# Kernel tuning notes

Hardware: AMD Instinct MI355X
Metric: run time of the kernel (lower is better)

## Reference

```python
import jax, jax.numpy as jnp
import numpy as np
import math

N = 50000      # nodes
E = 800000     # edges
IN = 64        # in_channels
HID = 128      # hidden_channels
OUT = 64       # out_channels
RATIO = 0.8
K = int(math.ceil(RATIO * N))  # 40000 nodes kept after TopKPooling


def setup_inputs() -> dict:
    key = jax.random.key(0)
    ks = jax.random.split(key, 12)
    x = jax.random.normal(ks[0], (N, IN), jnp.float32)
    edge_index = jax.random.randint(ks[1], (2, E), 0, N, dtype=jnp.int32)
    batch = jnp.zeros((N,), jnp.int32)  # single graph

    def glorot(k, fi, fo):
        return jax.random.normal(k, (fi, fo), jnp.float32) * (1.0 / np.sqrt(fi))

    W1 = glorot(ks[2], IN, HID);  b1 = jnp.zeros((HID,), jnp.float32)
    pool_w = jax.random.normal(ks[3], (HID,), jnp.float32) * (1.0 / np.sqrt(HID))
    W2 = glorot(ks[4], HID, OUT); b2 = jnp.zeros((OUT,), jnp.float32)
    W3 = glorot(ks[5], OUT, HID); b3 = jnp.zeros((HID,), jnp.float32)
    W4 = glorot(ks[6], HID, IN);  b4 = jnp.zeros((IN,), jnp.float32)
    return dict(x=x, edge_index=edge_index, batch=batch,
                W1=W1, b1=b1, pool_w=pool_w, W2=W2, b2=b2,
                W3=W3, b3=b3, W4=W4, b4=b4)


def gcn_conv(x, src, dst, ew, W, b, n):
    """PyG GCNConv: D^{-1/2}(A+I)D^{-1/2} X W + b; ew is a 0/1 edge mask."""
    h = x @ W                                             # [n, d_out]
    deg = 1.0 + jax.ops.segment_sum(ew, dst, num_segments=n)  # self-loop adds 1
    dis = jax.lax.rsqrt(deg)
    norm = dis[src] * dis[dst] * ew                       # [E]
    agg = jax.ops.segment_sum(norm[:, None] * h[src], dst, num_segments=n)
    agg = agg + h * (dis * dis)[:, None]                  # self-loop: norm = 1/deg
    return agg + b


def reference(x, edge_index, batch, W1, b1, pool_w, W2, b2, W3, b3, W4, b4):
    src, dst = edge_index[0], edge_index[1]
    ew = jnp.ones((E,), x.dtype)

    # conv1 + relu
    h = jax.nn.relu(gcn_conv(x, src, dst, ew, W1, b1, N))

    # TopKPooling(ratio=0.8): score = tanh(x.w/||w||), keep top-K, scale x by score
    score = jnp.tanh(h @ pool_w / jnp.linalg.norm(pool_w))  # [N]
    vals, perm = jax.lax.top_k(score, K)
    hp = h[perm] * vals[:, None]                            # [K, HID]
    # remap edges to pooled node ids; drop edges touching removed nodes via mask
    new_idx = jnp.full((N,), -1, jnp.int32).at[perm].set(jnp.arange(K, dtype=jnp.int32))
    ns, nd = new_idx[src], new_idx[dst]
    valid = ((ns >= 0) & (nd >= 0)).astype(x.dtype)
    ns = jnp.maximum(ns, 0)
    nd = jnp.maximum(nd, 0)

    h2 = jax.nn.relu(gcn_conv(hp, ns, nd, valid, W2, b2, K))
    h3 = jax.nn.relu(gcn_conv(h2, ns, nd, valid, W3, b3, K))
    h4 = gcn_conv(h3, ns, nd, valid, W4, b4, K)             # [K, IN]

    # global_mean_pool over the (single) graph -> [1, IN]
    return jnp.mean(h4, axis=0, keepdims=True)
```

## Files before the change

### kernel.cpp

```cpp
#include <hip/hip_runtime.h>
#include <hip/hip_bf16.h>
#include <stdint.h>

#define N_NODES 50000
#define N_EDGES 800000
#define K_KEEP  40000
#define BKT     196
#define BCAP    6144

typedef unsigned long long u64;
typedef unsigned int u32;
typedef unsigned short u16;
typedef __hip_bfloat16 bf16;
typedef __hip_bfloat162 bf16x2;
typedef __attribute__((ext_vector_type(8))) short short8;
typedef __attribute__((ext_vector_type(8))) unsigned short ushort8;
typedef __attribute__((ext_vector_type(4))) float f32x4;

struct Ctl {
  u64 prefix;
  u32 kremain;
  u32 cnt;
  float inv_norm;
  u32 isfp32;
  u32 done;
  u32 pad;
  u32 gen;
  u32 done2;
  u32 hist[256];
};

__device__ __forceinline__ float bf2f(bf16 v) { return __bfloat162float(v); }
__device__ __forceinline__ float bfbits2f(unsigned short u) {
  return __uint_as_float(((u32)u) << 16);
}
__device__ __forceinline__ float loadF(const void* p, size_t i, bool f32) {
  return f32 ? ((const float*)p)[i] : bf2f(((const bf16*)p)[i]);
}
__device__ __forceinline__ short f2bf_bits(float f) {
  bf16 t = __float2bfloat16(f);
  return *(const short*)&t;
}

__device__ __forceinline__ void gather_row8_pre(const ushort8* __restrict__ H, int d, int lane,
                                                const int* __restrict__ rowstart,
                                                const int* __restrict__ len,
                                                const int* __restrict__ csr,
                                                float* acc)
{
  ushort8 v = H[(size_t)d * 8 + lane];
  #pragma unroll
  for (int c = 0; c < 8; ++c) acc[c] = bfbits2f(v[c]);
  int i = rowstart[d];
  int i1 = len ? (i + len[d]) : rowstart[d + 1];
  for (; i + 8 <= i1; i += 8) {
    int s0 = csr[i],     s1 = csr[i + 1], s2 = csr[i + 2], s3 = csr[i + 3];
    int s4 = csr[i + 4], s5 = csr[i + 5], s6 = csr[i + 6], s7 = csr[i + 7];
    ushort8 v0 = H[(size_t)s0 * 8 + lane];
    ushort8 v1 = H[(size_t)s1 * 8 + lane];
    ushort8 v2 = H[(size_t)s2 * 8 + lane];
    ushort8 v3 = H[(size_t)s3 * 8 + lane];
    ushort8 v4 = H[(size_t)s4 * 8 + lane];
    ushort8 v5 = H[(size_t)s5 * 8 + lane];
    ushort8 v6 = H[(size_t)s6 * 8 + lane];
    ushort8 v7 = H[(size_t)s7 * 8 + lane];
    #pragma unroll
    for (int c = 0; c < 8; ++c) {
      acc[c] += (bfbits2f(v0[c]) + bfbits2f(v1[c]))
              + (bfbits2f(v2[c]) + bfbits2f(v3[c]));
      acc[c] += (bfbits2f(v4[c]) + bfbits2f(v5[c]))
              + (bfbits2f(v6[c]) + bfbits2f(v7[c]));
    }
  }
  for (; i + 4 <= i1; i += 4) {
    int s0 = csr[i], s1 = csr[i + 1], s2 = csr[i + 2], s3 = csr[i + 3];
    ushort8 v0 = H[(size_t)s0 * 8 + lane];
    ushort8 v1 = H[(size_t)s1 * 8 + lane];
    ushort8 v2 = H[(size_t)s2 * 8 + lane];
    ushort8 v3 = H[(size_t)s3 * 8 + lane];
    #pragma unroll
    for (int c = 0; c < 8; ++c) {
      acc[c] += (bfbits2f(v0[c]) + bfbits2f(v1[c]))
              + (bfbits2f(v2[c]) + bfbits2f(v3[c]));
    }
  }
  for (; i < i1; ++i) {
    int s = csr[i];
    ushort8 vv = H[(size_t)s * 8 + lane];
    #pragma unroll
    for (int c = 0; c < 8; ++c) acc[c] += bfbits2f(vv[c]);
  }
}

__device__ __forceinline__ void gather_wave_partial(const ushort8* __restrict__ H, int d,
                                                    int slot, int unit,
                                                    const int* __restrict__ rowstart,
                                                    const int* __restrict__ len,
                                                    const int* __restrict__ csr,
                                                    float* acc)
{
  #pragma unroll
  for (int c = 0; c < 8; ++c) acc[c] = 0.f;
  if (slot == 0) {
    ushort8 v = H[(size_t)d * 8 + unit];
    #pragma unroll
    for (int c = 0; c < 8; ++c) acc[c] = bfbits2f(v[c]);
  }
  int i0 = rowstart[d];
  int i1 = i0 + len[d];
  int i = i0 + slot;
  for (; i + 8 < i1; i += 16) {
    int sa = csr[i], sb = csr[i + 8];
    ushort8 va = H[(size_t)sa * 8 + unit];
    ushort8 vb = H[(size_t)sb * 8 + unit];
    #pragma unroll
    for (int c = 0; c < 8; ++c) acc[c] += bfbits2f(va[c]) + bfbits2f(vb[c]);
  }
  if (i < i1) {
    int s = csr[i];
    ushort8 vv = H[(size_t)s * 8 + unit];
    #pragma unroll
    for (int c = 0; c < 8; ++c) acc[c] += bfbits2f(vv[c]);
  }
}


__global__ void init_kernel(const unsigned short* __restrict__ x16,
                            int* __restrict__ bucket_cur, int* __restrict__ detcnt, Ctl* ctl) {
  __shared__ u32 dsh[256];
  int i = blockIdx.x * 256 + threadIdx.x;
  if (i < BKT) bucket_cur[i] = i * BCAP;
  if (blockIdx.x == 0) {
    ctl->hist[threadIdx.x] = 0u;
    if (threadIdx.x == 0) {
      ctl->prefix = 0ull; ctl->kremain = K_KEEP; ctl->cnt = 0u;
      ctl->done = 0u; ctl->pad = 0u; ctl->gen = 0u; ctl->done2 = 0u;
    }
  }
  if (blockIdx.x < 64) {
    int base = blockIdx.x * 2048;
    u32 c = 0;
    for (int j = threadIdx.x; j < 2048; j += 256) {
      u32 h = x16[base + j];
      if ((h & 0x7F80u) == 0x7F80u) c++;
    }
    dsh[threadIdx.x] = c;
    __syncthreads();
    for (int s = 128; s > 0; s >>= 1) {
      if (threadIdx.x < s) dsh[threadIdx.x] += dsh[threadIdx.x + s];
      __syncthreads();
    }
    if (threadIdx.x == 0) detcnt[blockIdx.x] = (int)dsh[0];
  }
}


__global__ void bucket_scatter_kernel(const int* __restrict__ src, const int* __restrict__ dst,
                                      int* __restrict__ bucket_cur, u32* __restrict__ bucketbuf,
                                      const int* __restrict__ detcnt, const void* __restrict__ pw,
                                      Ctl* ctl)
{
  __shared__ u32 hist[BKT];
  __shared__ u32 base[BKT];
  __shared__ int f32sh;
  __shared__ float ns[128];
  const int tid = threadIdx.x;
  const int e0 = blockIdx.x * 2048;

  if (tid < 64) {
    int dc = detcnt[tid];
    for (int off = 32; off; off >>= 1) dc += __shfl_down(dc, off);
    if (tid == 0) f32sh = (dc >= 16) ? 1 : 0;
  }
  for (int t = tid; t < BKT; t += 256) hist[t] = 0;
  __syncthreads();
  const bool f32in = f32sh != 0;

  int dreg[8], sreg[8];
  #pragma unroll
  for (int j = 0; j < 8; ++j) {
    int e = e0 + j * 256 + tid;
    if (e < N_EDGES) { dreg[j] = dst[e]; sreg[j] = src[e]; }
    else             { dreg[j] = -1;     sreg[j] = 0;      }
  }
  #pragma unroll
  for (int j = 0; j < 8; ++j)
    if (dreg[j] >= 0) atomicAdd(&hist[dreg[j] >> 8], 1u);
  __syncthreads();
  for (int t = tid; t < BKT; t += 256) {
    u32 c = hist[t];
    base[t] = c ? (u32)atomicAdd(&bucket_cur[t], (int)c) : 0u;
    hist[t] = 0;
  }
  __syncthreads();
  #pragma unroll
  for (int j = 0; j < 8; ++j) {
    if (dreg[j] >= 0) {
      int d = dreg[j];
      int b = d >> 8;
      u32 pos = base[b] + atomicAdd(&hist[b], 1u);
      bucketbuf[pos] = ((u32)sreg[j] << 8) | (u32)(d & 255);
    }
  }
  if (blockIdx.x == 0) {
    if (tid < 128) { float v = loadF(pw, tid, f32in); ns[tid] = v * v; }
    __syncthreads();
    for (int s = 64; s > 0; s >>= 1) {
      if (tid < s) ns[tid] += ns[tid + s];
      __syncthreads();
    }
    if (tid == 0) {
      ctl->inv_norm = 1.0f / sqrtf(ns[0]);
      ctl->isfp32 = f32in ? 1u : 0u;
    }
  }
}


__global__ void csr_from_buckets_kernel(const u32* __restrict__ bucketbuf, const int* __restrict__ bucket_cur,
                                        int* __restrict__ rowstart, float* __restrict__ dis,
                                        int* __restrict__ csr,
                                        const void* __restrict__ x, ushort8* __restrict__ xbf,
                                        const Ctl* __restrict__ ctl)
{
  __shared__ u32 cnt[256];
  __shared__ u32 loc[256];
  __shared__ u32 cur[256];
  __shared__ float disS[256];
  const int b = blockIdx.x;
  const int tid = threadIdx.x;

  int v = (tid < BKT) ? (bucket_cur[tid] - tid * BCAP) : 0;
  loc[tid] = (u32)v;
  __syncthreads();
  for (int off = 1; off < 256; off <<= 1) {
    u32 t = (tid >= off) ? loc[tid - off] : 0;
    __syncthreads();
    loc[tid] += t;
    __syncthreads();
  }
  const int bc = bucket_cur[b] - b * BCAP;
  const int off0 = (int)loc[b] - bc;
  if (b == BKT - 1 && tid == 0) rowstart[N_NODES] = (int)loc[BKT - 1];
  __syncthreads();

  const u32* buf = bucketbuf + (size_t)b * BCAP;
  cnt[tid] = 0;
  __syncthreads();
  for (int i = tid; i < bc; i += 256) atomicAdd(&cnt[buf[i] & 255u], 1u);
  __syncthreads();
  u32 c = cnt[tid];
  loc[tid] = c;
  __syncthreads();
  for (int off = 1; off < 256; off <<= 1) {
    u32 t = (tid >= off) ? loc[tid - off] : 0;
    __syncthreads();
    loc[tid] += t;
    __syncthreads();
  }
  int node = b * 256 + tid;
  u32 excl = loc[tid] - c;
  float ddv = rsqrtf(1.0f + (float)c);
  disS[tid] = ddv;
  if (node < N_NODES) {
    rowstart[node] = off0 + (int)excl;
    dis[node] = ddv;
  }
  cur[tid] = off0 + excl;
  __syncthreads();
  for (int i = tid; i < bc; i += 256) {
    u32 p = buf[i];
    u32 pos = atomicAdd(&cur[p & 255u], 1u);
    csr[pos] = (int)(p >> 8);
  }
  {
    const bool f32in = ctl->isfp32 != 0;
    if (f32in) {
      const float* xf = (const float*)x;
      for (int u = tid; u < 2048; u += 256) {
        int r = u >> 3, lane = u & 7;
        int d = b * 256 + r;
        if (d < N_NODES) {
          float sc = disS[r];
          ushort8 o;
          #pragma unroll
          for (int c2 = 0; c2 < 8; ++c2)
            o[c2] = (u16)f2bf_bits(xf[(size_t)d * 64 + lane * 8 + c2] * sc);
          xbf[(size_t)d * 8 + lane] = o;
        }
      }
    } else {
      const ushort8* xi = (const ushort8*)x;
      for (int u = tid; u < 2048; u += 256) {
        int r = u >> 3, lane = u & 7;
        int d = b * 256 + r;
        if (d < N_NODES) {
          float sc = disS[r];
          ushort8 vv = xi[(size_t)d * 8 + lane];
          ushort8 o;
          #pragma unroll
          for (int c2 = 0; c2 < 8; ++c2)
            o[c2] = (u16)f2bf_bits(bfbits2f(vv[c2]) * sc);
          xbf[(size_t)d * 8 + lane] = o;
        }
      }
    }
  }
}


__global__ void gather_h2_kernel(const bf16* __restrict__ P, const int* __restrict__ rowstart,
                                 const int* __restrict__ len, const int* __restrict__ csr,
                                 const float* __restrict__ dis,
                                 const void* __restrict__ b, const Ctl* __restrict__ ctl,
                                 bf16* __restrict__ P2, int M)
{
  const bool f32 = ctl->isfp32 != 0;
  const int tid = threadIdx.x;
  const int d = blockIdx.x * 4 + (tid >> 6);
  const int lane = tid & 63;
  const int slot = lane >> 3, unit = lane & 7;
  const ushort8* H = (const ushort8*)P;
  float acc[8];
  gather_wave_partial(H, d, slot, unit, rowstart, len, csr, acc);
  #pragma unroll
  for (int m = 8; m < 64; m <<= 1)
    #pragma unroll
    for (int c = 0; c < 8; ++c) acc[c] += __shfl_xor(acc[c], m);
  if (slot == 0) {
    float dd = dis[d];
    ushort8 outv;
    #pragma unroll
    for (int c = 0; c < 8; ++c) {
      float h = acc[c] * dd + loadF(b, 8 * unit + c, f32);
      outv[c] = (u16)f2bf_bits(fmaxf(h, 0.f) * dd);
    }
    ((ushort8*)P2)[(size_t)d * 8 + unit] = outv;
  }
}


__global__ void gemm_in_kernel(const ushort8* __restrict__ xbf,
                               const int* __restrict__ rowstart, const int* __restrict__ csr,
                               const float* __restrict__ dis,
                               const void* __restrict__ W, const void* __restrict__ b,
                               const void* __restrict__ pw,
                               bf16* __restrict__ Y, const Ctl* __restrict__ ctl,
                               float* __restrict__ score, u64* __restrict__ keys)
{
  __shared__ short Xs[64 * 72];
  __shared__ short Wt[128 * 72];
  __shared__ float bs[128];
  __shared__ float ps[128];
  const bool f32 = ctl->isfp32 != 0;
  const int tid = threadIdx.x;
  const int row0 = blockIdx.x * 64;

  if (!f32) {
    const short8* W8 = (const short8*)W;
    for (int i = tid; i < 1024; i += 256) {
      int k = i >> 4, nb = i & 15;
      short8 v = W8[i];
      #pragma unroll
      for (int j = 0; j < 8; ++j) Wt[(nb * 8 + j) * 72 + k] = v[j];
    }
  } else {
    for (int i = tid; i < 64 * 128; i += 256) {
      int k = i >> 7, n = i & 127;
      Wt[n * 72 + k] = f2bf_bits(((const float*)W)[i]);
    }
  }
  for (int u = tid; u < 512; u += 256) {
    int r = u >> 3, lane = u & 7;
    int d = row0 + r;
    float acc[8];
    short8 outv;
    if (d < N_NODES) {
      gather_row8_pre(xbf, d, lane, rowstart, nullptr, csr, acc);
      float dd = dis[d];
      #pragma unroll
      for (int c = 0; c < 8; ++c) outv[c] = f2bf_bits(acc[c] * dd);
    } else {
      #pragma unroll
      for (int c = 0; c < 8; ++c) outv[c] = 0;
    }
    *(short8*)&Xs[r * 72 + lane * 8] = outv;
  }
  for (int i = tid; i < 128; i += 256) { bs[i] = loadF(b, i, f32); ps[i] = loadF(pw, i, f32); }
  __syncthreads();

  const int lane = tid & 63;
  const int w = tid >> 6;
  const int l16 = lane & 15;
  const int quad = lane >> 4;
  f32x4 acc[8];
  #pragma unroll
  for (int ct = 0; ct < 8; ++ct) acc[ct] = (f32x4){0.f, 0.f, 0.f, 0.f};
  const int arow = w * 16 + l16;
  #pragma unroll
  for (int kc = 0; kc < 2; ++kc) {
    short8 a = *(short8*)&Xs[arow * 72 + kc * 32 + quad * 8];
    #pragma unroll
    for (int ct = 0; ct < 8; ++ct) {
      short8 bb = *(short8*)&Wt[(ct * 16 + l16) * 72 + kc * 32 + quad * 8];
      acc[ct] = __builtin_amdgcn_mfma_f32_16x16x32_bf16(a, bb, acc[ct], 0, 0, 0);
    }
  }
  float inv_norm = ctl->inv_norm;
  #pragma unroll
  for (int r = 0; r < 4; ++r) {
    int gr = row0 + w * 16 + quad * 4 + r;
    float p = 0.f;
    #pragma unroll
    for (int ct = 0; ct < 8; ++ct) {
      int col = ct * 16 + l16;
      float h = acc[ct][r] + bs[col];
      if (gr < N_NODES) Y[(size_t)gr * 128 + col] = __float2bfloat16(h);
      p += fmaxf(h, 0.f) * ps[col];
    }
    p += __shfl_down(p, 8, 16);
    p += __shfl_down(p, 4, 16);
    p += __shfl_down(p, 2, 16);
    p += __shfl_down(p, 1, 16);
    if (l16 == 0 && gr < N_NODES) {
      float sc = tanhf(p * inv_norm);
      score[gr] = sc;
      u32 u = __float_as_uint(sc);
      u = (u & 0x80000000u) ? ~u : (u | 0x80000000u);
      keys[gr] = (((u64)u) << 16) | (u64)(0xFFFFu - (u32)gr);
    }
  }
}

__global__ void gemm_128_64_kernel(const bf16* __restrict__ X, const void* __restrict__ W,
                                   bf16* __restrict__ Y, const Ctl* __restrict__ ctl,
                                   int M, int relu_x,
                                   const int* __restrict__ kept, const float* __restrict__ score,
                                   const float* __restrict__ prescale)
{
  __shared__ short Xs[64 * 136];
  __shared__ short Wt[64 * 136];
  __shared__ int keptS[64];
  __shared__ float scS[64];
  const bool f32 = ctl->isfp32 != 0;
  const int tid = threadIdx.x;
  const int row0 = blockIdx.x * 64;

  if (kept) {
    for (int i = tid; i < 64; i += 256) {
      int o = kept[row0 + i];
      keptS[i] = o;
      scS[i] = score[o];
    }
  }
  __syncthreads();

  if (!f32) {
    const short8* W8 = (const short8*)W;
    for (int i = tid; i < 1024; i += 256) {
      int k = i >> 3, nb = i & 7;
      short8 v = W8[i];
      #pragma unroll
      for (int j = 0; j < 8; ++j) Wt[(nb * 8 + j) * 136 + k] = v[j];
    }
  } else {
    for (int i = tid; i < 128 * 64; i += 256) {
      int k = i >> 6, n = i & 63;
      Wt[n * 136 + k] = f2bf_bits(((const float*)W)[i]);
    }
  }
  const u32* X2 = (const u32*)X;
  for (int p = tid; p < 64 * 64; p += 256) {
    int r = p >> 6, kp = p & 63;
    int srow = kept ? keptS[r] : (row0 + r);
    u32 v = X2[(size_t)srow * 64 + kp];
    if (relu_x) {
      if (v & 0x8000u) v &= 0xFFFF0000u;
      if (v & 0x80000000u) v &= 0x0000FFFFu;
    }
    if (kept) {
      bf16x2 h = *(bf16x2*)&v;
      float s = scS[r];
      bf16x2 o;
      o.x = __float2bfloat16(fmaxf(bf2f(h.x), 0.f) * s);
      o.y = __float2bfloat16(fmaxf(bf2f(h.y), 0.f) * s);
      v = *(u32*)&o;
    }
    *(u32*)&Xs[r * 136 + 2 * kp] = v;
  }
  __syncthreads();

  const int lane = tid & 63;
  const int w = tid >> 6;
  const int l16 = lane & 15;
  const int quad = lane >> 4;
  f32x4 acc[4];
  #pragma unroll
  for (int ct = 0; ct < 4; ++ct) acc[ct] = (f32x4){0.f, 0.f, 0.f, 0.f};
  const int arow = w * 16 + l16;
  #pragma unroll
  for (int kc = 0; kc < 4; ++kc) {
    short8 a = *(short8*)&Xs[arow * 136 + kc * 32 + quad * 8];
    #pragma unroll
    for (int ct = 0; ct < 4; ++ct) {
      short8 bb = *(short8*)&Wt[(ct * 16 + l16) * 136 + kc * 32 + quad * 8];
      acc[ct] = __builtin_amdgcn_mfma_f32_16x16x32_bf16(a, bb, acc[ct], 0, 0, 0);
    }
  }
  #pragma unroll
  for (int ct = 0; ct < 4; ++ct)
    #pragma unroll
    for (int r = 0; r < 4; ++r) {
      int gr = row0 + w * 16 + quad * 4 + r;
      float val = acc[ct][r];
      if (prescale) val *= prescale[gr];
      Y[(size_t)gr * 64 + ct * 16 + l16] = __float2bfloat16(val);
    }
}

__global__ void gemm_64_128_kernel(const bf16* __restrict__ P2,
                                   const int* __restrict__ rowstart, const int* __restrict__ len,
                                   const int* __restrict__ csr, const float* __restrict__ dis,
                                   const void* __restrict__ W, const void* __restrict__ b,
                                   bf16* __restrict__ Y, const Ctl* __restrict__ ctl, int M)
{
  __shared__ short Xs[64 * 72];
  __shared__ short Wt[128 * 72];
  __shared__ float bs[128];
  const bool f32 = ctl->isfp32 != 0;
  const int tid = threadIdx.x;
  const int row0 = blockIdx.x * 64;

  if (!f32) {
    const short8* W8 = (const short8*)W;
    for (int i = tid; i < 1024; i += 256) {
      int k = i >> 4, nb = i & 15;
      short8 v = W8[i];
      #pragma unroll
      for (int j = 0; j < 8; ++j) Wt[(nb * 8 + j) * 72 + k] = v[j];
    }
  } else {
    for (int i = tid; i < 64 * 128; i += 256) {
      int k = i >> 7, n = i & 127;
      Wt[n * 72 + k] = f2bf_bits(((const float*)W)[i]);
    }
  }
  {
    const ushort8* H = (const ushort8*)P2;
    for (int u = tid; u < 512; u += 256) {
      int r = u >> 3, lane = u & 7;
      int d = row0 + r;
      float acc[8];
      gather_row8_pre(H, d, lane, rowstart, len, csr, acc);
      float dd = dis[d];
      short8 outv;
      #pragma unroll
      for (int c = 0; c < 8; ++c) outv[c] = f2bf_bits(acc[c] * dd);
      *(short8*)&Xs[r * 72 + lane * 8] = outv;
    }
  }
  for (int i = tid; i < 128; i += 256) bs[i] = loadF(b, i, f32);
  __syncthreads();

  const int lane = tid & 63;
  const int w = tid >> 6;
  const int l16 = lane & 15;
  const int quad = lane >> 4;
  f32x4 acc[8];
  #pragma unroll
  for (int ct = 0; ct < 8; ++ct) acc[ct] = (f32x4){0.f, 0.f, 0.f, 0.f};
  const int arow = w * 16 + l16;
  #pragma unroll
  for (int kc = 0; kc < 2; ++kc) {
    short8 a = *(short8*)&Xs[arow * 72 + kc * 32 + quad * 8];
    #pragma unroll
    for (int ct = 0; ct < 8; ++ct) {
      short8 bb = *(short8*)&Wt[(ct * 16 + l16) * 72 + kc * 32 + quad * 8];
      acc[ct] = __builtin_amdgcn_mfma_f32_16x16x32_bf16(a, bb, acc[ct], 0, 0, 0);
    }
  }
  #pragma unroll
  for (int ct = 0; ct < 8; ++ct)
    #pragma unroll
    for (int r = 0; r < 4; ++r) {
      int gr = row0 + w * 16 + quad * 4 + r;
      int col = ct * 16 + l16;
      Y[(size_t)gr * 128 + col] = __float2bfloat16(acc[ct][r] + bs[col]);
    }
}

__global__ void agg_gather64_final_kernel(const bf16* __restrict__ P, const int* __restrict__ rowstart,
                                          const int* __restrict__ len, const int* __restrict__ csr,
                                          const float* __restrict__ dis,
                                          float* __restrict__ partial, int M, int nblk)
{
  __shared__ float cs[64];
  const int tid = threadIdx.x;
  if (tid < 64) cs[tid] = 0.f;
  __syncthreads();
  const int lane = tid & 63;
  const int slot = lane >> 3, unit = lane & 7;
  const int wave = tid >> 6;
  const ushort8* H = (const ushort8*)P;
  float acc[8];
  #pragma unroll
  for (int c = 0; c < 8; ++c) acc[c] = 0.f;
  for (int d = blockIdx.x * 4 + wave; d < M; d += nblk * 4) {
    float part[8];
    gather_wave_partial(H, d, slot, unit, rowstart, len, csr, part);
    float dd = dis[d];
    #pragma unroll
    for (int c = 0; c < 8; ++c) acc[c] += part[c] * dd;
  }
  #pragma unroll
  for (int c = 0; c < 8; ++c) atomicAdd(&cs[8 * unit + c], acc[c]);
  __syncthreads();
  if (tid < 64) partial[(size_t)tid * nblk + blockIdx.x] = cs[tid];
}

__global__ void reduce_out_kernel(const float* __restrict__ partial, const void* __restrict__ b,
                                  const Ctl* __restrict__ ctl, void* __restrict__ out, int nblk)
{
  __shared__ float sh[256];
  int c = blockIdx.x;
  float s = 0.f;
  for (int j = threadIdx.x; j < nblk; j += 256) s += partial[(size_t)c * nblk + j];
  sh[threadIdx.x] = s;
  __syncthreads();
  for (int st = 128; st > 0; st >>= 1) {
    if (threadIdx.x < st) sh[threadIdx.x] += sh[threadIdx.x + st];
    __syncthreads();
  }
  if (threadIdx.x == 0) {
    const bool f32 = ctl->isfp32 != 0;
    float val = sh[0] / (float)K_KEEP + loadF(b, c, f32);
    if (f32) ((float*)out)[c] = val;
    else     ((bf16*)out)[c] = __float2bfloat16(val);
  }
}


__device__ __forceinline__ void mark_slice(const u64* __restrict__ keys, Ctl* ctl,
                                           int* __restrict__ new_idx, int* __restrict__ kept,
                                           int i)
{
  if (i >= N_NODES) return;
  if (keys[i] >= ctl->prefix) {
    int pos = (int)atomicAdd(&ctl->cnt, 1u);
    new_idx[i] = pos;
    kept[pos] = i;
  } else {
    new_idx[i] = -1;
  }
}

__global__ void histpick_kernel(const u64* __restrict__ keys, Ctl* ctl, int shift, int pass,
                                int nblocks, int* __restrict__ new_idx, int* __restrict__ kept) {
  __shared__ u32 lh[256];
  __shared__ u32 sfx[256];
  __shared__ int lastflag;
  __shared__ int selsh;
  const int tid = threadIdx.x;
  const u32 g = ctl->gen;
  if (g != 0u) {
    if ((u32)pass == g)
      mark_slice(keys, ctl, new_idx, kept, blockIdx.x * 256 + tid);
    return;
  }
  lh[tid] = 0;
  __syncthreads();
  u64 prefix = ctl->prefix;
  int i = blockIdx.x * 256 + tid;
  if (i < N_NODES) {
    u64 key = keys[i];
    if ((key >> (shift + 8)) == (prefix >> (shift + 8)))
      atomicAdd(&lh[(u32)((key >> shift) & 0xFF)], 1u);
  }
  __syncthreads();
  u32 c = lh[tid];
  if (c) atomicAdd(&ctl->hist[tid], c);
  __syncthreads();
  if (tid == 0) {
    __threadfence();
    u32 old = atomicAdd(&ctl->done, 1u);
    lastflag = (old == (u32)(nblocks - 1));
  }
  __syncthreads();
  if (!lastflag) return;
  u32 cc = atomicExch(&ctl->hist[tid], 0u);
  sfx[tid] = cc;
  __syncthreads();
  for (int off = 1; off < 256; off <<= 1) {
    u32 t = (tid + off < 256) ? sfx[tid + off] : 0u;
    __syncthreads();
    sfx[tid] += t;
    __syncthreads();
  }
  u32 kr = ctl->kremain;
  u32 above = (tid < 255) ? sfx[tid + 1] : 0u;
  if (sfx[tid] >= kr && above < kr) selsh = tid;
  __syncthreads();
  if (tid == 0) {
    int sel = selsh;
    u32 ab = (sel < 255) ? sfx[sel + 1] : 0u;
    u32 newkr = kr - ab;
    u32 bucketcnt = sfx[sel] - ab;
    ctl->kremain = newkr;
    ctl->prefix = prefix | (((u64)(u32)sel) << shift);
    if (newkr == bucketcnt) ctl->gen = (u32)(pass + 1);
    ctl->done = 0u;
  }
}

__global__ void mark_kernel(const u64* __restrict__ keys, Ctl* ctl,
                            int* __restrict__ new_idx, int* __restrict__ kept)
{
  u32 g = ctl->gen;
  if (g >= 1u && g <= 5u) return;
  mark_slice(keys, ctl, new_idx, kept, blockIdx.x * 256 + (int)threadIdx.x);
}


__global__ void csr2_build_kernel(const int* __restrict__ kept, const int* __restrict__ rowstart1,
                                  const int* __restrict__ csr1, const int* __restrict__ new_idx,
                                  Ctl* ctl, int* __restrict__ rowstart2, int* __restrict__ len2,
                                  float* __restrict__ dis2, int* __restrict__ csr2)
{
  int kp = blockIdx.x * 256 + threadIdx.x;
  int lane = threadIdx.x & 63;
  int c = 0;
  int i0 = 0, i1 = 0;
  if (kp < K_KEEP) {
    int o = kept[kp];
    i0 = rowstart1[o]; i1 = rowstart1[o + 1];
    int i = i0;
    for (; i + 4 <= i1; i += 4) {
      int s0 = csr1[i], s1 = csr1[i + 1], s2 = csr1[i + 2], s3 = csr1[i + 3];
      c += (new_idx[s0] >= 0) + (new_idx[s1] >= 0) + (new_idx[s2] >= 0) + (new_idx[s3] >= 0);
    }
    for (; i < i1; ++i) c += (new_idx[csr1[i]] >= 0);
  }
  int pre = c;
  #pragma unroll
  for (int off = 1; off < 64; off <<= 1) {
    int t = __shfl_up(pre, off);
    if (lane >= off) pre += t;
  }
  int wtot = __shfl(pre, 63);
  int wbase = 0;
  if (lane == 0) wbase = (int)atomicAdd(&ctl->pad, (u32)wtot);
  wbase = __shfl(wbase, 0);
  int base = wbase + pre - c;
  if (kp < K_KEEP) {
    rowstart2[kp] = base;
    len2[kp] = c;
    dis2[kp] = rsqrtf(1.0f + (float)c);
    int w = base;
    for (int i = i0; i < i1; ++i) {
      int ns = new_idx[csr1[i]];
      if (ns >= 0) csr2[w++] = ns;
    }
  }
}


extern "C" void kernel_launch(void* const* d_in, const int* in_sizes, int n_in,
                              void* d_out, int out_size, void* d_ws, size_t ws_size,
                              hipStream_t stream)
{
  const void* x  = d_in[0];
  const int*  ei = (const int*)d_in[1];
  const void* W1 = d_in[3];
  const void* b1 = d_in[4];
  const void* pw = d_in[5];
  const void* W2 = d_in[6];
  const void* b2 = d_in[7];
  const void* W3 = d_in[8];
  const void* b3 = d_in[9];
  const void* W4 = d_in[10];
  const void* b4 = d_in[11];

  const int* src = ei;
  const int* dst = ei + N_EDGES;

  float* F = (float*)d_ws;
  bf16*  A16       = (bf16*)F;
  bf16*  B16       = (bf16*)(F + 3200000);
  bf16*  C16       = (bf16*)(F + 6400000);
  u32*   xbf       = (u32*)(F + 9000000);
  float* dis1      = F + 10600000;
  float* dis2      = F + 10650000;
  float* score     = F + 10690000;
  u64*   keys      = (u64*)(F + 10740000);
  int*   new_idx   = (int*)(F + 10840000);
  int*   kept      = (int*)(F + 10890000);
  int*   len2      = (int*)(F + 10930000);
  int*   rowstart1 = (int*)(F + 10970000);
  int*   rowstart2 = (int*)(F + 11020004);
  int*   csr1      = (int*)(F + 11060008);
  int*   csr2      = (int*)(F + 11860008);
  Ctl*   ctl       = (Ctl*)(F + 12660008);
  int*   detcnt    = (int*)(F + 12660856);
  int*   bucket_cur= (int*)(F + 12660920);
  u32*   bucketbuf = (u32*)(F + 12726908);
  float* partial   = F + 13931132;

  const int NB1 = (N_NODES + 255) / 256;
  const int EB2 = (N_EDGES + 2047) / 2048;
  const int GB1 = (N_NODES + 63) / 64;
  const int WBK = K_KEEP / 4;
  const int CB2 = (K_KEEP + 255) / 256;
  const int NBF = 1024;

  init_kernel<<<NB1, 256, 0, stream>>>((const unsigned short*)x, bucket_cur, detcnt, ctl);

  bucket_scatter_kernel<<<EB2, 256, 0, stream>>>(src, dst, bucket_cur, bucketbuf,
                                                 detcnt, pw, ctl);
  csr_from_buckets_kernel<<<BKT, 256, 0, stream>>>(bucketbuf, bucket_cur, rowstart1, dis1, csr1,
                                                   x, (ushort8*)xbf, ctl);

  gemm_in_kernel<<<GB1, 256, 0, stream>>>((const ushort8*)xbf, rowstart1, csr1, dis1,
                                          W1, b1, pw, B16, ctl, score, keys);

  for (int p = 0; p < 6; ++p)
    histpick_kernel<<<NB1, 256, 0, stream>>>(keys, ctl, 40 - 8 * p, p, NB1, new_idx, kept);
  mark_kernel<<<NB1, 256, 0, stream>>>(keys, ctl, new_idx, kept);

  csr2_build_kernel<<<CB2, 256, 0, stream>>>(kept, rowstart1, csr1, new_idx, ctl,
                                             rowstart2, len2, dis2, csr2);

  gemm_128_64_kernel<<<K_KEEP / 64, 256, 0, stream>>>(B16, W2, A16, ctl, K_KEEP, 0, kept, score, dis2);
  gather_h2_kernel<<<WBK, 256, 0, stream>>>(A16, rowstart2, len2, csr2, dis2, b2, ctl, C16, K_KEEP);

  gemm_64_128_kernel<<<K_KEEP / 64, 256, 0, stream>>>(C16, rowstart2, len2, csr2, dis2,
                                                      W3, b3, B16, ctl, K_KEEP);

  gemm_128_64_kernel<<<K_KEEP / 64, 256, 0, stream>>>(B16, W4, A16, ctl, K_KEEP, 1, nullptr, nullptr, dis2);
  agg_gather64_final_kernel<<<NBF, 256, 0, stream>>>(A16, rowstart2, len2, csr2, dis2,
                                                     partial, K_KEEP, NBF);
  reduce_out_kernel<<<64, 256, 0, stream>>>(partial, b4, ctl, d_out, NBF);
}
```

Measured before the change: 305.2 us.

## Use 12-bit radix passes for top-k selection and vectorize edge loads

```diff
diff --git a/kernel.cpp b/kernel.cpp
--- a/kernel.cpp
+++ b/kernel.cpp
@@ -7,6 +7,8 @@
 #define K_KEEP  40000
 #define BKT     196
 #define BCAP    6144
+#define RBITS   12
+#define RBINS   4096
 
 typedef unsigned long long u64;
 typedef unsigned int u32;
@@ -126,16 +128,15 @@
 
 
 __global__ void init_kernel(const unsigned short* __restrict__ x16,
-                            int* __restrict__ bucket_cur, int* __restrict__ detcnt, Ctl* ctl) {
+                            int* __restrict__ bucket_cur, int* __restrict__ detcnt,
+                            Ctl* ctl, u32* __restrict__ hist4k) {
   __shared__ u32 dsh[256];
   int i = blockIdx.x * 256 + threadIdx.x;
   if (i < BKT) bucket_cur[i] = i * BCAP;
-  if (blockIdx.x == 0) {
-    ctl->hist[threadIdx.x] = 0u;
-    if (threadIdx.x == 0) {
-      ctl->prefix = 0ull; ctl->kremain = K_KEEP; ctl->cnt = 0u;
-      ctl->done = 0u; ctl->pad = 0u; ctl->gen = 0u; ctl->done2 = 0u;
-    }
+  if (i < RBINS) hist4k[i] = 0u;
+  if (blockIdx.x == 0 && threadIdx.x == 0) {
+    ctl->prefix = 0ull; ctl->kremain = K_KEEP; ctl->cnt = 0u;
+    ctl->done = 0u; ctl->pad = 0u; ctl->gen = 0u; ctl->done2 = 0u;
   }
   if (blockIdx.x < 64) {
     int base = blockIdx.x * 2048;
@@ -177,11 +178,23 @@
   const bool f32in = f32sh != 0;
 
   int dreg[8], sreg[8];
-  #pragma unroll
-  for (int j = 0; j < 8; ++j) {
-    int e = e0 + j * 256 + tid;
-    if (e < N_EDGES) { dreg[j] = dst[e]; sreg[j] = src[e]; }
-    else             { dreg[j] = -1;     sreg[j] = 0;      }
+  const int eb = e0 + tid * 8;
+  if (e0 + 2048 <= N_EDGES) {
+    const int4* d4 = (const int4*)(dst + eb);
+    const int4* s4 = (const int4*)(src + eb);
+    int4 da = d4[0], db = d4[1];
+    int4 sa = s4[0], sb = s4[1];
+    dreg[0] = da.x; dreg[1] = da.y; dreg[2] = da.z; dreg[3] = da.w;
+    dreg[4] = db.x; dreg[5] = db.y; dreg[6] = db.z; dreg[7] = db.w;
+    sreg[0] = sa.x; sreg[1] = sa.y; sreg[2] = sa.z; sreg[3] = sa.w;
+    sreg[4] = sb.x; sreg[5] = sb.y; sreg[6] = sb.z; sreg[7] = sb.w;
+  } else {
+    #pragma unroll
+    for (int j = 0; j < 8; ++j) {
+      int e = eb + j;
+      if (e < N_EDGES) { dreg[j] = dst[e]; sreg[j] = src[e]; }
+      else             { dreg[j] = -1;     sreg[j] = 0;      }
+    }
   }
   #pragma unroll
   for (int j = 0; j < 8; ++j)
@@ -654,12 +667,12 @@
   }
 }
 
-__global__ void histpick_kernel(const u64* __restrict__ keys, Ctl* ctl, int shift, int pass,
-                                int nblocks, int* __restrict__ new_idx, int* __restrict__ kept) {
-  __shared__ u32 lh[256];
+__global__ void histpick_kernel(const u64* __restrict__ keys, Ctl* ctl, u32* __restrict__ hist4k,
+                                int shift, int pass, int nblocks,
+                                int* __restrict__ new_idx, int* __restrict__ kept) {
+  __shared__ u32 lh[RBINS];
   __shared__ u32 sfx[256];
   __shared__ int lastflag;
-  __shared__ int selsh;
   const int tid = threadIdx.x;
   const u32 g = ctl->gen;
   if (g != 0u) {
@@ -667,18 +680,21 @@
       mark_slice(keys, ctl, new_idx, kept, blockIdx.x * 256 + tid);
     return;
   }
-  lh[tid] = 0;
+  #pragma unroll
+  for (int j = 0; j < RBINS / 256; ++j) lh[tid + j * 256] = 0;
   __syncthreads();
   u64 prefix = ctl->prefix;
   int i = blockIdx.x * 256 + tid;
   if (i < N_NODES) {
     u64 key = keys[i];
-    if ((key >> (shift + 8)) == (prefix >> (shift + 8)))
-      atomicAdd(&lh[(u32)((key >> shift) & 0xFF)], 1u);
-  }
-  __syncthreads();
-  u32 c = lh[tid];
-  if (c) atomicAdd(&ctl->hist[tid], c);
+    if ((key >> (shift + RBITS)) == (prefix >> (shift + RBITS)))
+      atomicAdd(&lh[(u32)((key >> shift) & (RBINS - 1))], 1u);
+  }
+  __syncthreads();
+  for (int bb = tid; bb < RBINS; bb += 256) {
+    u32 c = lh[bb];
+    if (c) atomicAdd(&hist4k[bb], c);
+  }
   __syncthreads();
   if (tid == 0) {
     __threadfence();
@@ -687,8 +703,18 @@
   }
   __syncthreads();
   if (!lastflag) return;
-  u32 cc = atomicExch(&ctl->hist[tid], 0u);
-  sfx[tid] = cc;
+  u32 cnt[16];
+  u32 loc[16];
+  {
+    u32 tot = 0;
+    #pragma unroll
+    for (int j = 15; j >= 0; --j) {
+      cnt[j] = atomicExch(&hist4k[tid * 16 + j], 0u);
+      tot += cnt[j];
+      loc[j] = tot;
+    }
+    sfx[tid] = tot;
+  }
   __syncthreads();
   for (int off = 1; off < 256; off <<= 1) {
     u32 t = (tid + off < 256) ? sfx[tid + off] : 0u;
@@ -697,18 +723,19 @@
     __syncthreads();
   }
   u32 kr = ctl->kremain;
-  u32 above = (tid < 255) ? sfx[tid + 1] : 0u;
-  if (sfx[tid] >= kr && above < kr) selsh = tid;
-  __syncthreads();
-  if (tid == 0) {
-    int sel = selsh;
-    u32 ab = (sel < 255) ? sfx[sel + 1] : 0u;
-    u32 newkr = kr - ab;
-    u32 bucketcnt = sfx[sel] - ab;
-    ctl->kremain = newkr;
-    ctl->prefix = prefix | (((u64)(u32)sel) << shift);
-    if (newkr == bucketcnt) ctl->gen = (u32)(pass + 1);
-    ctl->done = 0u;
+  u32 above_chunks = (tid < 255) ? sfx[tid + 1] : 0u;
+  #pragma unroll
+  for (int j = 0; j < 16; ++j) {
+    u32 gs  = loc[j] + above_chunks;
+    u32 gs1 = ((j < 15) ? loc[j + 1] : 0u) + above_chunks;
+    if (gs >= kr && gs1 < kr) {
+      int sel = tid * 16 + j;
+      u32 newkr = kr - gs1;
+      ctl->kremain = newkr;
+      ctl->prefix = prefix | (((u64)(u32)sel) << shift);
+      if (newkr == cnt[j]) ctl->gen = (u32)(pass + 1);
+      ctl->done = 0u;
+    }
   }
 }
 
@@ -716,7 +743,7 @@
                             int* __restrict__ new_idx, int* __restrict__ kept)
 {
   u32 g = ctl->gen;
-  if (g >= 1u && g <= 5u) return;
+  if (g >= 1u && g <= 3u) return;
   mark_slice(keys, ctl, new_idx, kept, blockIdx.x * 256 + (int)threadIdx.x);
 }
 
@@ -802,6 +829,7 @@
   Ctl*   ctl       = (Ctl*)(F + 12660008);
   int*   detcnt    = (int*)(F + 12660856);
   int*   bucket_cur= (int*)(F + 12660920);
+  u32*   hist4k    = (u32*)(F + 12661120);
   u32*   bucketbuf = (u32*)(F + 12726908);
   float* partial   = F + 13931132;
 
@@ -812,7 +840,7 @@
   const int CB2 = (K_KEEP + 255) / 256;
   const int NBF = 1024;
 
-  init_kernel<<<NB1, 256, 0, stream>>>((const unsigned short*)x, bucket_cur, detcnt, ctl);
+  init_kernel<<<NB1, 256, 0, stream>>>((const unsigned short*)x, bucket_cur, detcnt, ctl, hist4k);
 
   bucket_scatter_kernel<<<EB2, 256, 0, stream>>>(src, dst, bucket_cur, bucketbuf,
                                                  detcnt, pw, ctl);
@@ -822,8 +850,9 @@
   gemm_in_kernel<<<GB1, 256, 0, stream>>>((const ushort8*)xbf, rowstart1, csr1, dis1,
                                           W1, b1, pw, B16, ctl, score, keys);
 
-  for (int p = 0; p < 6; ++p)
-    histpick_kernel<<<NB1, 256, 0, stream>>>(keys, ctl, 40 - 8 * p, p, NB1, new_idx, kept);
+  for (int p = 0; p < 4; ++p)
+    histpick_kernel<<<NB1, 256, 0, stream>>>(keys, ctl, hist4k, 36 - RBITS * p, p, NB1,
+                                             new_idx, kept);
   mark_kernel<<<NB1, 256, 0, stream>>>(keys, ctl, new_idx, kept);
 
   csr2_build_kernel<<<CB2, 256, 0, stream>>>(kept, rowstart1, csr1, new_idx, ctl,
```

Measured after the change: 307.2 us. No clear change (+0.6%).

## Collapse final GCN layer and mean pool into weighted column sum

Applied to the files above, without the earlier changes.

```diff
diff --git a/kernel.cpp b/kernel.cpp
--- a/kernel.cpp
+++ b/kernel.cpp
@@ -126,10 +126,12 @@
 
 
 __global__ void init_kernel(const unsigned short* __restrict__ x16,
-                            int* __restrict__ bucket_cur, int* __restrict__ detcnt, Ctl* ctl) {
+                            int* __restrict__ bucket_cur, int* __restrict__ detcnt,
+                            Ctl* ctl, float* __restrict__ cvec) {
   __shared__ u32 dsh[256];
   int i = blockIdx.x * 256 + threadIdx.x;
   if (i < BKT) bucket_cur[i] = i * BCAP;
+  if (i < K_KEEP) cvec[i] = 0.f;
   if (blockIdx.x == 0) {
     ctl->hist[threadIdx.x] = 0u;
     if (threadIdx.x == 0) {
@@ -177,11 +179,23 @@
   const bool f32in = f32sh != 0;
 
   int dreg[8], sreg[8];
-  #pragma unroll
-  for (int j = 0; j < 8; ++j) {
-    int e = e0 + j * 256 + tid;
-    if (e < N_EDGES) { dreg[j] = dst[e]; sreg[j] = src[e]; }
-    else             { dreg[j] = -1;     sreg[j] = 0;      }
+  const int eb = e0 + tid * 8;
+  if (e0 + 2048 <= N_EDGES) {
+    const int4* d4 = (const int4*)(dst + eb);
+    const int4* s4 = (const int4*)(src + eb);
+    int4 da = d4[0], db = d4[1];
+    int4 sa = s4[0], sb = s4[1];
+    dreg[0] = da.x; dreg[1] = da.y; dreg[2] = da.z; dreg[3] = da.w;
+    dreg[4] = db.x; dreg[5] = db.y; dreg[6] = db.z; dreg[7] = db.w;
+    sreg[0] = sa.x; sreg[1] = sa.y; sreg[2] = sa.z; sreg[3] = sa.w;
+    sreg[4] = sb.x; sreg[5] = sb.y; sreg[6] = sb.z; sreg[7] = sb.w;
+  } else {
+    #pragma unroll
+    for (int j = 0; j < 8; ++j) {
+      int e = eb + j;
+      if (e < N_EDGES) { dreg[j] = dst[e]; sreg[j] = src[e]; }
+      else             { dreg[j] = -1;     sreg[j] = 0;      }
+    }
   }
   #pragma unroll
   for (int j = 0; j < 8; ++j)
@@ -589,53 +603,51 @@
     }
 }
 
-__global__ void agg_gather64_final_kernel(const bf16* __restrict__ P, const int* __restrict__ rowstart,
-                                          const int* __restrict__ len, const int* __restrict__ csr,
-                                          const float* __restrict__ dis,
-                                          float* __restrict__ partial, int M, int nblk)
-{
-  __shared__ float cs[64];
+
+__global__ void weighted_sum_kernel(const bf16* __restrict__ H3, const float* __restrict__ cvec,
+                                    const float* __restrict__ dis,
+                                    float* __restrict__ partial, int M, int nblk)
+{
+  __shared__ float cs[128];
   const int tid = threadIdx.x;
-  if (tid < 64) cs[tid] = 0.f;
-  __syncthreads();
-  const int lane = tid & 63;
-  const int slot = lane >> 3, unit = lane & 7;
-  const int wave = tid >> 6;
-  const ushort8* H = (const ushort8*)P;
+  if (tid < 128) cs[tid] = 0.f;
+  __syncthreads();
+  const int lane = tid & 15;
+  const ushort8* H = (const ushort8*)H3;
   float acc[8];
   #pragma unroll
   for (int c = 0; c < 8; ++c) acc[c] = 0.f;
-  for (int d = blockIdx.x * 4 + wave; d < M; d += nblk * 4) {
-    float part[8];
-    gather_wave_partial(H, d, slot, unit, rowstart, len, csr, part);
-    float dd = dis[d];
-    #pragma unroll
-    for (int c = 0; c < 8; ++c) acc[c] += part[c] * dd;
-  }
-  #pragma unroll
-  for (int c = 0; c < 8; ++c) atomicAdd(&cs[8 * unit + c], acc[c]);
-  __syncthreads();
-  if (tid < 64) partial[(size_t)tid * nblk + blockIdx.x] = cs[tid];
-}
-
-__global__ void reduce_out_kernel(const float* __restrict__ partial, const void* __restrict__ b,
-                                  const Ctl* __restrict__ ctl, void* __restrict__ out, int nblk)
-{
-  __shared__ float sh[256];
-  int c = blockIdx.x;
-  float s = 0.f;
-  for (int j = threadIdx.x; j < nblk; j += 256) s += partial[(size_t)c * nblk + j];
-  sh[threadIdx.x] = s;
-  __syncthreads();
-  for (int st = 128; st > 0; st >>= 1) {
-    if (threadIdx.x < st) sh[threadIdx.x] += sh[threadIdx.x + st];
-    __syncthreads();
-  }
-  if (threadIdx.x == 0) {
+  for (int r = (blockIdx.x * 256 + tid) >> 4; r < M; r += nblk * 16) {
+    float wgt = dis[r] * cvec[r];
+    ushort8 v = H[(size_t)r * 16 + lane];
+    #pragma unroll
+    for (int c = 0; c < 8; ++c) acc[c] += wgt * fmaxf(bfbits2f(v[c]), 0.f);
+  }
+  #pragma unroll
+  for (int c = 0; c < 8; ++c) atomicAdd(&cs[8 * lane + c], acc[c]);
+  __syncthreads();
+  if (tid < 128) partial[(size_t)tid * nblk + blockIdx.x] = cs[tid];
+}
+
+__global__ void final_out_kernel(const float* __restrict__ partial, const void* __restrict__ W4,
+                                 const void* __restrict__ b4, const Ctl* __restrict__ ctl,
+                                 void* __restrict__ out, int nblk)
+{
+  __shared__ float S[128];
+  const int tid = threadIdx.x;
+  if (tid < 128) {
+    float s = 0.f;
+    for (int j = 0; j < nblk; ++j) s += partial[(size_t)tid * nblk + j];
+    S[tid] = s;
+  }
+  __syncthreads();
+  if (tid < 64) {
     const bool f32 = ctl->isfp32 != 0;
-    float val = sh[0] / (float)K_KEEP + loadF(b, c, f32);
-    if (f32) ((float*)out)[c] = val;
-    else     ((bf16*)out)[c] = __float2bfloat16(val);
+    float o = 0.f;
+    for (int k = 0; k < 128; ++k) o += S[k] * loadF(W4, (size_t)k * 64 + tid, f32);
+    float val = o / (float)K_KEEP + loadF(b4, tid, f32);
+    if (f32) ((float*)out)[tid] = val;
+    else     ((bf16*)out)[tid] = __float2bfloat16(val);
   }
 }
 
@@ -724,7 +736,8 @@
 __global__ void csr2_build_kernel(const int* __restrict__ kept, const int* __restrict__ rowstart1,
                                   const int* __restrict__ csr1, const int* __restrict__ new_idx,
                                   Ctl* ctl, int* __restrict__ rowstart2, int* __restrict__ len2,
-                                  float* __restrict__ dis2, int* __restrict__ csr2)
+                                  float* __restrict__ dis2, int* __restrict__ csr2,
+                                  float* __restrict__ cvec)
 {
   int kp = blockIdx.x * 256 + threadIdx.x;
   int lane = threadIdx.x & 63;
@@ -754,11 +767,16 @@
   if (kp < K_KEEP) {
     rowstart2[kp] = base;
     len2[kp] = c;
-    dis2[kp] = rsqrtf(1.0f + (float)c);
+    float ddv = rsqrtf(1.0f + (float)c);
+    dis2[kp] = ddv;
+    atomicAdd(&cvec[kp], ddv);
     int w = base;
     for (int i = i0; i < i1; ++i) {
       int ns = new_idx[csr1[i]];
-      if (ns >= 0) csr2[w++] = ns;
+      if (ns >= 0) {
+        csr2[w++] = ns;
+        atomicAdd(&cvec[ns], ddv);
+      }
     }
   }
 }
@@ -802,6 +820,7 @@
   Ctl*   ctl       = (Ctl*)(F + 12660008);
   int*   detcnt    = (int*)(F + 12660856);
   int*   bucket_cur= (int*)(F + 12660920);
+  float* cvec      = F + 12665216;
   u32*   bucketbuf = (u32*)(F + 12726908);
   float* partial   = F + 13931132;
 
@@ -810,9 +829,9 @@
   const int GB1 = (N_NODES + 63) / 64;
   const int WBK = K_KEEP / 4;
   const int CB2 = (K_KEEP + 255) / 256;
-  const int NBF = 1024;
-
-  init_kernel<<<NB1, 256, 0, stream>>>((const unsigned short*)x, bucket_cur, detcnt, ctl);
+  const int NWS = 512;
+
+  init_kernel<<<NB1, 256, 0, stream>>>((const unsigned short*)x, bucket_cur, detcnt, ctl, cvec);
 
   bucket_scatter_kernel<<<EB2, 256, 0, stream>>>(src, dst, bucket_cur, bucketbuf,
                                                  detcnt, pw, ctl);
@@ -827,7 +846,7 @@
   mark_kernel<<<NB1, 256, 0, stream>>>(keys, ctl, new_idx, kept);
 
   csr2_build_kernel<<<CB2, 256, 0, stream>>>(kept, rowstart1, csr1, new_idx, ctl,
-                                             rowstart2, len2, dis2, csr2);
+                                             rowstart2, len2, dis2, csr2, cvec);
 
   gemm_128_64_kernel<<<K_KEEP / 64, 256, 0, stream>>>(B16, W2, A16, ctl, K_KEEP, 0, kept, score, dis2);
   gather_h2_kernel<<<WBK, 256, 0, stream>>>(A16, rowstart2, len2, csr2, dis2, b2, ctl, C16, K_KEEP);
@@ -835,8 +854,6 @@
   gemm_64_128_kernel<<<K_KEEP / 64, 256, 0, stream>>>(C16, rowstart2, len2, csr2, dis2,
                                                       W3, b3, B16, ctl, K_KEEP);
 
-  gemm_128_64_kernel<<<K_KEEP / 64, 256, 0, stream>>>(B16, W4, A16, ctl, K_KEEP, 1, nullptr, nullptr, dis2);
-  agg_gather64_final_kernel<<<NBF, 256, 0, stream>>>(A16, rowstart2, len2, csr2, dis2,
-                                                     partial, K_KEEP, NBF);
-  reduce_out_kernel<<<64, 256, 0, stream>>>(partial, b4, ctl, d_out, NBF);
-}
+  weighted_sum_kernel<<<NWS, 256, 0, stream>>>(B16, cvec, dis2, partial, K_KEEP, NWS);
+  final_out_kernel<<<1, 256, 0, stream>>>(partial, W4, b4, ctl, d_out, NWS);
+}
```

Result: slower. 347.4 us (+13.9%).
